# Optimization experiments

Measured on AMD Instinct MI355X. Metric: run time of the kernel, lower is better.

The kernel has to match this reference:

```python
import jax, jax.numpy as jnp
import numpy as np

NUM_HEADS = 3

def setup_inputs() -> dict:
    key = jax.random.key(0)
    k0, k1, k2, k3, k4 = jax.random.split(key, 5)
    B, C, H, W = 2, 96, 64, 64
    N = H * W
    x = jax.random.normal(k0, (B, N, C), jnp.float32)
    # depthwise conv: groups=C, out_channels=3*C -> OIHW weight [3C, 1, 3, 3]
    qkv_w = jax.random.normal(k1, (3 * C, 1, 3, 3), jnp.float32) * 0.1
    qkv_b = jax.random.normal(k2, (3 * C,), jnp.float32) * 0.01
    proj_w = jax.random.normal(k3, (C, C), jnp.float32) * (1.0 / np.sqrt(C))
    proj_b = jax.random.normal(k4, (C,), jnp.float32) * 0.01
    return {"x": x, "qkv_w": qkv_w, "qkv_b": qkv_b,
            "proj_w": proj_w, "proj_b": proj_b, "H": H, "W": W}


def reference(x, qkv_w, qkv_b, proj_w, proj_b, H, W):
    B, N, C = x.shape
    h = NUM_HEADS
    d = C // h
    scale = d ** (-0.5)
    # [B,N,C] -> [B,C,H,W]
    x2d = jnp.transpose(x, (0, 2, 1)).reshape(B, C, H, W)
    # depthwise conv, 'SAME' padding (padding = kernel//2, stride 1)
    qkv = jax.lax.conv_general_dilated(
        x2d, qkv_w, window_strides=(1, 1), padding="SAME",
        feature_group_count=C,
        dimension_numbers=("NCHW", "OIHW", "NCHW"))
    qkv = qkv + qkv_b[None, :, None, None]
    qkv = qkv.reshape(B, 3, h, d, H * W)  # same channel split as torch reshape
    q, k, v = qkv[:, 0], qkv[:, 1], qkv[:, 2]  # each [B,h,d,N]
    # attn = q^T @ k  (q,k permuted to [B,h,N,d] in the original)
    attn = jnp.einsum("bhdn,bhdm->bhnm", q, k) * scale  # [B,h,N,N]
    attn = jax.nn.softmax(attn, axis=-1)
    out = jnp.einsum("bhnm,bhdm->bhnd", attn, v)  # [B,h,N,d]
    # replicate torch: transpose(2,3) -> [B,h,d,N], reshape(B, N, C)
    out = jnp.transpose(out, (0, 1, 3, 2)).reshape(B, H * W, C)
    out = out @ proj_w.T + proj_b
    return out
```

## Files before the change

kernel.cpp:

```cpp
#include <hip/hip_runtime.h>
#include <hip/hip_bf16.h>

typedef short bf16x8 __attribute__((ext_vector_type(8)));
typedef float f32x4 __attribute__((ext_vector_type(4)));
typedef unsigned int u32x4 __attribute__((ext_vector_type(4)));

#define B_ 2
#define C_ 96
#define N_ 4096
#define NH_ 3
#define DH_ 32
#define BH_ 6
#define KSPLIT 2
#define TQ 64
#define MQ 4
#define TK 64
#define WAVES_PER_BLOCK 4
#define KT_PER_WAVE (N_ / KSPLIT / WAVES_PER_BLOCK / TK)


__global__ __launch_bounds__(256) void conv_qkv(
    const float* __restrict__ x, const float* __restrict__ qw,
    const float* __restrict__ qb, __hip_bfloat16* __restrict__ q_b,
    __hip_bfloat16* __restrict__ k_b, __hip_bfloat16* __restrict__ vT) {
  __shared__ float xs[18 * 64];
  int b = blockIdx.x / C_;
  int cin = blockIdx.x % C_;
  int y0 = blockIdx.y * 16;
  int yl0 = (y0 == 0) ? 0 : y0 - 1;
  int yl1 = (y0 + 16 > 63) ? 63 : y0 + 16;
  int nload = (yl1 - yl0 + 1) * 64;
  const float* xp = x + (size_t)b * N_ * C_ + cin;
  for (int i = threadIdx.x; i < nload; i += 256)
    xs[i] = xp[(size_t)(yl0 * 64 + i) * C_];
  __syncthreads();

  int s = cin >> 5;
  int cl = cin & 31;
  float w[3][9], bias[3];
#pragma unroll
  for (int r = 0; r < 3; ++r) {
    int o = 3 * cin + r;
#pragma unroll
    for (int t = 0; t < 9; ++t) w[r][t] = qw[o * 9 + t];
    bias[r] = qb[o];
  }
  const float scale = 0.2550349f;
  float mul = (s == 0) ? scale : 1.0f;
  __hip_bfloat16* base_[3];
  int dd_[3];
#pragma unroll
  for (int r = 0; r < 3; ++r) {
    int c = 3 * cl + r, head = c >> 5, dd = c & 31, bh = b * NH_ + head;
    dd_[r] = dd;
    if (s == 2)
      base_[r] = vT + (size_t)bh * N_ * DH_;
    else if (s == 1)
      base_[r] = k_b + (size_t)bh * N_ * DH_;
    else
      base_[r] = q_b + (size_t)bh * N_ * DH_;
  }

  for (int i = threadIdx.x; i < 1024; i += 256) {
    int y = y0 + (i >> 6), xx = i & 63;
    float a0 = bias[0], a1 = bias[1], a2 = bias[2];
#pragma unroll
    for (int dy = 0; dy < 3; ++dy) {
      int ry = y + dy - 1;
      if ((unsigned)ry >= 64u) continue;
#pragma unroll
      for (int dx = 0; dx < 3; ++dx) {
        int rx = xx + dx - 1;
        if ((unsigned)rx >= 64u) continue;
        float xv = xs[(ry - yl0) * 64 + rx];
        a0 += w[0][dy * 3 + dx] * xv;
        a1 += w[1][dy * 3 + dx] * xv;
        a2 += w[2][dy * 3 + dx] * xv;
      }
    }
    int n = y * 64 + xx;
    float av[3] = {a0 * mul, a1 * mul, a2 * mul};
#pragma unroll
    for (int r = 0; r < 3; ++r) {
      int off;
      if (s == 0)
        off = n * DH_ + dd_[r];
      else if (s == 1)
        off = ((n >> 6) << 11) | (((n >> 4) & 3) << 9) | ((n & 15) << 5) | dd_[r];
      else {
        int kap = (((n >> 2) & 3) << 3) | (((n >> 4) & 1) << 2) | (n & 3);
        off = ((n >> 6) << 11) | (((n >> 5) & 1) << 10) | (dd_[r] << 5) | kap;
      }
      base_[r][off] = __float2bfloat16(av[r]);
    }
  }
}

__global__ __launch_bounds__(256, 2) void attn_fwd(
    const __hip_bfloat16* __restrict__ q_b, const __hip_bfloat16* __restrict__ k_b,
    const __hip_bfloat16* __restrict__ vT, float* __restrict__ Opart,
    float* __restrict__ lpart) {
  __shared__ __align__(16) float Tm[WAVES_PER_BLOCK][32 * 65];
  __shared__ float l_s[WAVES_PER_BLOCK][TQ];
  int qt = blockIdx.x, ks = blockIdx.y, bh = blockIdx.z;
  int tid = threadIdx.x;
  int lane = tid & 63, wave = tid >> 6;
  int c = lane & 15, quad = lane >> 4;

  const __hip_bfloat16* qbase = q_b + ((size_t)bh * N_ + qt * TQ) * DH_;
  bf16x8 qa[MQ];
#pragma unroll
  for (int m = 0; m < MQ; ++m)
    qa[m] = *(const bf16x8*)(qbase + (m * 16 + c) * DH_ + quad * 8);

  f32x4 oT[2][MQ];
  f32x4 lacT[MQ];
#pragma unroll
  for (int m = 0; m < MQ; ++m) {
    lacT[m] = (f32x4){0.f, 0.f, 0.f, 0.f};
#pragma unroll
    for (int n0 = 0; n0 < 2; ++n0) oT[n0][m] = (f32x4){0.f, 0.f, 0.f, 0.f};
  }
  bf16x8 ones;
  {
    short v = (c == 0) ? (short)0x3F80 : (short)0;
    ones = (bf16x8){v, v, v, v, v, v, v, v};
  }

  const __hip_bfloat16* kb = k_b + (size_t)bh * N_ * DH_;
  const __hip_bfloat16* vb = vT + (size_t)bh * N_ * DH_;
  int key0 = ks * (N_ / KSPLIT) + wave * (N_ / KSPLIT / WAVES_PER_BLOCK);

  bf16x8 kf[2][4];
  {
    size_t tb0 = (size_t)key0 * DH_;
#pragma unroll
    for (int t = 0; t < 4; ++t)
      kf[0][t] = *(const bf16x8*)(kb + tb0 + t * 512 + c * 32 + quad * 8);
  }

#pragma unroll
  for (int kt = 0; kt < KT_PER_WAVE; ++kt) {
    const int cur = kt & 1, nxt = cur ^ 1;
    size_t tbase = (size_t)(key0 + kt * TK) * DH_;

    if (kt + 1 < KT_PER_WAVE) {
      size_t tnext = (size_t)(key0 + (kt + 1) * TK) * DH_;
#pragma unroll
      for (int t = 0; t < 4; ++t)
        kf[nxt][t] = *(const bf16x8*)(kb + tnext + t * 512 + c * 32 + quad * 8);
    }

    bf16x8 vf[2][2];
#pragma unroll
    for (int n0 = 0; n0 < 2; ++n0)
#pragma unroll
      for (int h = 0; h < 2; ++h)
        vf[n0][h] = *(const bf16x8*)(vb + tbase + h * 1024 + (n0 * 16 + c) * 32 + quad * 8);

#pragma unroll
    for (int m = 0; m < MQ; ++m) {
      f32x4 pT[4];
      f32x4 z = {0.f, 0.f, 0.f, 0.f};
#pragma unroll
      for (int t = 0; t < 4; ++t)
        pT[t] = __builtin_amdgcn_mfma_f32_16x16x32_bf16(kf[cur][t], qa[m], z, 0, 0, 0);

#pragma unroll
      for (int t = 0; t < 4; ++t)
#pragma unroll
        for (int r = 0; r < 4; ++r)
          pT[t][r] = __builtin_amdgcn_exp2f(pT[t][r]);

      unsigned wv[4][2];
#pragma unroll
      for (int t = 0; t < 4; ++t) {
        unsigned h0 = __builtin_bit_cast(unsigned short, __float2bfloat16(pT[t][0]));
        unsigned h1 = __builtin_bit_cast(unsigned short, __float2bfloat16(pT[t][1]));
        unsigned h2 = __builtin_bit_cast(unsigned short, __float2bfloat16(pT[t][2]));
        unsigned h3 = __builtin_bit_cast(unsigned short, __float2bfloat16(pT[t][3]));
        wv[t][0] = h0 | (h1 << 16);
        wv[t][1] = h2 | (h3 << 16);
      }
#pragma unroll
      for (int h = 0; h < 2; ++h) {
        u32x4 bw = {wv[2 * h][0], wv[2 * h][1], wv[2 * h + 1][0], wv[2 * h + 1][1]};
        bf16x8 pB = __builtin_bit_cast(bf16x8, bw);
        oT[0][m] = __builtin_amdgcn_mfma_f32_16x16x32_bf16(vf[0][h], pB, oT[0][m], 0, 0, 0);
        oT[1][m] = __builtin_amdgcn_mfma_f32_16x16x32_bf16(vf[1][h], pB, oT[1][m], 0, 0, 0);
        lacT[m] = __builtin_amdgcn_mfma_f32_16x16x32_bf16(ones, pB, lacT[m], 0, 0, 0);
      }
    }
  }

  float* T = Tm[wave];
#pragma unroll
  for (int n0 = 0; n0 < 2; ++n0)
#pragma unroll
    for (int m = 0; m < MQ; ++m)
#pragma unroll
      for (int r = 0; r < 4; ++r)
        T[(n0 * 16 + quad * 4 + r) * 65 + m * 16 + c] = oT[n0][m][r];
  if (lane < 16) {
#pragma unroll
    for (int m = 0; m < MQ; ++m) l_s[wave][m * 16 + lane] = lacT[m][0];
  }
  __syncthreads();

  int nbase = qt * TQ;
  float* Ob = Opart + (size_t)(ks * BH_ + bh) * DH_ * N_ + nbase;
  const float* Sf = (const float*)Tm;
#pragma unroll
  for (int it = 0; it < 8; ++it) {
    int idx = it * 256 + tid;
    int dd = idx >> 6, q = idx & 63;
    float s = Sf[0 * 2080 + dd * 65 + q] + Sf[1 * 2080 + dd * 65 + q] +
              Sf[2 * 2080 + dd * 65 + q] + Sf[3 * 2080 + dd * 65 + q];
    Ob[(size_t)dd * N_ + q] = s;
  }
  if (tid < TQ) {
    float s = l_s[0][tid] + l_s[1][tid] + l_s[2][tid] + l_s[3][tid];
    lpart[(size_t)(ks * BH_ + bh) * N_ + nbase + tid] = s;
  }
}

__global__ __launch_bounds__(256) void proj_out(
    const float* __restrict__ Opart, const float* __restrict__ lpart,
    const float* __restrict__ pw, const float* __restrict__ pb,
    float* __restrict__ out) {
  __shared__ float Wt[C_][100];
  __shared__ float Pt[16][100];
  __shared__ float bias[C_];
  int tid = threadIdx.x;
  for (int i = tid; i < C_ * C_; i += 256) Wt[i / C_][i % C_] = pw[i];
  if (tid < C_) bias[tid] = pb[tid];
  int row0 = blockIdx.x * 16;
  for (int i = tid; i < 16 * C_; i += 256) {
    int r = i / C_, cc = i % C_;
    int g = row0 + r;
    int b = g >> 12;
    int f = (g & 4095) * C_ + cc;
    int hh = f >> 17;
    int n = f & 4095;
    float osum = 0.f, lsum = 0.f;
    size_t obase = (size_t)g * C_ + cc;
    size_t lbase = (size_t)(b * NH_ + hh) * N_ + n;
#pragma unroll
    for (int ksq = 0; ksq < KSPLIT; ++ksq) {
      osum += Opart[(size_t)ksq * (BH_ * DH_ * N_) + obase];
      lsum += lpart[(size_t)ksq * (BH_ * N_) + lbase];
    }
    Pt[r][cc] = osum / lsum;
  }
  __syncthreads();

  int row = tid >> 4, cg = tid & 15;
  float acc[6] = {};
  for (int kk = 0; kk < C_; kk += 4) {
    f32x4 pv = *(const f32x4*)&Pt[row][kk];
    f32x4 wv[6];
#pragma unroll
    for (int i2 = 0; i2 < 6; ++i2) wv[i2] = *(const f32x4*)&Wt[cg * 6 + i2][kk];
#pragma unroll
    for (int i2 = 0; i2 < 6; ++i2)
      acc[i2] += pv[0] * wv[i2][0] + pv[1] * wv[i2][1] +
                 pv[2] * wv[i2][2] + pv[3] * wv[i2][3];
  }
#pragma unroll
  for (int i2 = 0; i2 < 6; ++i2)
    out[(size_t)(row0 + row) * C_ + cg * 6 + i2] = acc[i2] + bias[cg * 6 + i2];
}

extern "C" void kernel_launch(void* const* d_in, const int* in_sizes, int n_in,
                              void* d_out, int out_size, void* d_ws, size_t ws_size,
                              hipStream_t stream) {
  const float* x = (const float*)d_in[0];
  const float* qw = (const float*)d_in[1];
  const float* qb = (const float*)d_in[2];
  const float* pw = (const float*)d_in[3];
  const float* pb = (const float*)d_in[4];

  char* ws = (char*)d_ws;
  __hip_bfloat16* q_b = (__hip_bfloat16*)(ws);
  __hip_bfloat16* k_b = (__hip_bfloat16*)(ws + 1572864);
  __hip_bfloat16* vT = (__hip_bfloat16*)(ws + 3145728);
  float* Opart = (float*)(ws + 4718592);
  float* lpart = (float*)(ws + 11010048);

  hipLaunchKernelGGL(conv_qkv, dim3(B_ * C_, 4), dim3(256), 0, stream, x, qw, qb, q_b, k_b, vT);
  hipLaunchKernelGGL(attn_fwd, dim3(N_ / TQ, KSPLIT, BH_), dim3(256), 0, stream,
                     q_b, k_b, vT, Opart, lpart);
  hipLaunchKernelGGL(proj_out, dim3((B_ * N_) / 16, 1), dim3(256), 0, stream,
                     Opart, lpart, pw, pb, (float*)d_out);
}
```

Before: 118.2 us.

## Give each wave its own query tile and split keys eight ways across blocks

The attention kernel previously split one 64-query tile's keys across the four waves of a block and reduced their partial outputs through shared memory with a barrier. Now each wave owns a separate 64-query tile, the block covers 256 queries, and the key dimension is split into eight chunks across the grid. Each wave writes its partial output and row sums straight to global memory, so the shared-memory staging and the block barrier are gone. The cost is four times as many partial buffers: the workspace grows and the projection kernel has more partial results to write and then read back.

```diff
diff --git a/kernel.cpp b/kernel.cpp
--- a/kernel.cpp
+++ b/kernel.cpp
@@ -11,12 +11,12 @@
 #define NH_ 3
 #define DH_ 32
 #define BH_ 6
-#define KSPLIT 2
-#define TQ 64
+#define KSPLIT 8
+#define TQB 256
 #define MQ 4
 #define TK 64
 #define WAVES_PER_BLOCK 4
-#define KT_PER_WAVE (N_ / KSPLIT / WAVES_PER_BLOCK / TK)
+#define KT_PER_BLOCK (N_ / KSPLIT / TK)
 
 
 __global__ __launch_bounds__(256) void conv_qkv(
@@ -100,14 +100,13 @@
     const __hip_bfloat16* __restrict__ q_b, const __hip_bfloat16* __restrict__ k_b,
     const __hip_bfloat16* __restrict__ vT, float* __restrict__ Opart,
     float* __restrict__ lpart) {
-  __shared__ __align__(16) float Tm[WAVES_PER_BLOCK][32 * 65];
-  __shared__ float l_s[WAVES_PER_BLOCK][TQ];
   int qt = blockIdx.x, ks = blockIdx.y, bh = blockIdx.z;
   int tid = threadIdx.x;
   int lane = tid & 63, wave = tid >> 6;
   int c = lane & 15, quad = lane >> 4;
 
-  const __hip_bfloat16* qbase = q_b + ((size_t)bh * N_ + qt * TQ) * DH_;
+  int q0 = qt * TQB + wave * 64;
+  const __hip_bfloat16* qbase = q_b + ((size_t)bh * N_ + q0) * DH_;
   bf16x8 qa[MQ];
 #pragma unroll
   for (int m = 0; m < MQ; ++m)
@@ -129,7 +128,7 @@
 
   const __hip_bfloat16* kb = k_b + (size_t)bh * N_ * DH_;
   const __hip_bfloat16* vb = vT + (size_t)bh * N_ * DH_;
-  int key0 = ks * (N_ / KSPLIT) + wave * (N_ / KSPLIT / WAVES_PER_BLOCK);
+  int key0 = ks * (N_ / KSPLIT);
 
   bf16x8 kf[2][4];
   {
@@ -140,11 +139,11 @@
   }
 
 #pragma unroll
-  for (int kt = 0; kt < KT_PER_WAVE; ++kt) {
+  for (int kt = 0; kt < KT_PER_BLOCK; ++kt) {
     const int cur = kt & 1, nxt = cur ^ 1;
     size_t tbase = (size_t)(key0 + kt * TK) * DH_;
 
-    if (kt + 1 < KT_PER_WAVE) {
+    if (kt + 1 < KT_PER_BLOCK) {
       size_t tnext = (size_t)(key0 + (kt + 1) * TK) * DH_;
 #pragma unroll
       for (int t = 0; t < 4; ++t)
@@ -193,34 +192,18 @@
     }
   }
 
-  float* T = Tm[wave];
+  float* Ob = Opart + (size_t)(ks * BH_ + bh) * DH_ * N_ + q0;
 #pragma unroll
   for (int n0 = 0; n0 < 2; ++n0)
 #pragma unroll
     for (int m = 0; m < MQ; ++m)
 #pragma unroll
       for (int r = 0; r < 4; ++r)
-        T[(n0 * 16 + quad * 4 + r) * 65 + m * 16 + c] = oT[n0][m][r];
+        Ob[(size_t)(n0 * 16 + quad * 4 + r) * N_ + m * 16 + c] = oT[n0][m][r];
   if (lane < 16) {
-#pragma unroll
-    for (int m = 0; m < MQ; ++m) l_s[wave][m * 16 + lane] = lacT[m][0];
-  }
-  __syncthreads();
-
-  int nbase = qt * TQ;
-  float* Ob = Opart + (size_t)(ks * BH_ + bh) * DH_ * N_ + nbase;
-  const float* Sf = (const float*)Tm;
-#pragma unroll
-  for (int it = 0; it < 8; ++it) {
-    int idx = it * 256 + tid;
-    int dd = idx >> 6, q = idx & 63;
-    float s = Sf[0 * 2080 + dd * 65 + q] + Sf[1 * 2080 + dd * 65 + q] +
-              Sf[2 * 2080 + dd * 65 + q] + Sf[3 * 2080 + dd * 65 + q];
-    Ob[(size_t)dd * N_ + q] = s;
-  }
-  if (tid < TQ) {
-    float s = l_s[0][tid] + l_s[1][tid] + l_s[2][tid] + l_s[3][tid];
-    lpart[(size_t)(ks * BH_ + bh) * N_ + nbase + tid] = s;
+    float* lb = lpart + (size_t)(ks * BH_ + bh) * N_ + q0;
+#pragma unroll
+    for (int m = 0; m < MQ; ++m) lb[m * 16 + lane] = lacT[m][0];
   }
 }
 
@@ -285,10 +268,10 @@
   __hip_bfloat16* k_b = (__hip_bfloat16*)(ws + 1572864);
   __hip_bfloat16* vT = (__hip_bfloat16*)(ws + 3145728);
   float* Opart = (float*)(ws + 4718592);
-  float* lpart = (float*)(ws + 11010048);
+  float* lpart = (float*)(ws + 29884416);
 
   hipLaunchKernelGGL(conv_qkv, dim3(B_ * C_, 4), dim3(256), 0, stream, x, qw, qb, q_b, k_b, vT);
-  hipLaunchKernelGGL(attn_fwd, dim3(N_ / TQ, KSPLIT, BH_), dim3(256), 0, stream,
+  hipLaunchKernelGGL(attn_fwd, dim3(N_ / TQB, KSPLIT, BH_), dim3(256), 0, stream,
                      q_b, k_b, vT, Opart, lpart);
   hipLaunchKernelGGL(proj_out, dim3((B_ * N_) / 16, 1), dim3(256), 0, stream,
                      Opart, lpart, pw, pb, (float*)d_out);
```

After: 123.9 us. +4.9%, slower.
